# Kernel optimization log

Measured on AMD Instinct MI355X. Metric: run time of the kernel, lower is better.

## Reference

```python
import jax, jax.numpy as jnp
import numpy as np

B, T, H, L = 256, 1024, 64, 5  # batch, seq_len, hidden_size, num_layers


def setup_inputs() -> dict:
    key = jax.random.key(0)
    ks = jax.random.split(key, 10)
    s = 1.0 / np.sqrt(H)  # PyTorch LSTM/Linear uniform init bound

    def u(k, shape):
        return jax.random.uniform(k, shape, jnp.float32, -s, s)

    return {
        "x": jax.random.normal(ks[0], (B, T, 1), jnp.float32),
        "w_ih0": u(ks[1], (4 * H, 1)),          # layer 0 input weights (input_size=1)
        "w_ih_rest": u(ks[2], (L - 1, 4 * H, H)),  # layers 1..4 input weights
        "w_hh": u(ks[3], (L, 4 * H, H)),
        "b_ih": u(ks[4], (L, 4 * H)),
        "b_hh": u(ks[5], (L, 4 * H)),
        "W1": u(ks[6], (H, H)),
        "b1": u(ks[7], (H,)),
        "W2": u(ks[8], (1, H)),
        "b2": u(ks[9], (1,)),
        "future": 0,
    }


def _lstm_layer(x, w_ih, w_hh, b_ih, b_hh):
    # x: [B, T, in]; PyTorch gate order i, f, g, o
    gx = jnp.einsum('bti,gi->btg', x, w_ih) + b_ih  # precompute input projections [B,T,4H]
    h0 = jnp.zeros((x.shape[0], w_hh.shape[1]), x.dtype)

    def step(carry, gxt):
        h, c = carry
        gates = gxt + h @ w_hh.T + b_hh  # [B,4H]
        i, f, g, o = jnp.split(gates, 4, axis=-1)
        c = jax.nn.sigmoid(f) * c + jax.nn.sigmoid(i) * jnp.tanh(g)
        h = jax.nn.sigmoid(o) * jnp.tanh(c)
        return (h, c), h

    _, hs = jax.lax.scan(step, (h0, h0), jnp.swapaxes(gx, 0, 1))  # scan over time
    return jnp.swapaxes(hs, 0, 1)  # [B,T,H]


def _model(x, w_ih0, w_ih_rest, w_hh, b_ih, b_hh, W1, b1, W2, b2):
    # 5-layer LSTM (inter-layer dropout=0.1 is inactive in eval mode)
    h = _lstm_layer(x, w_ih0, w_hh[0], b_ih[0], b_hh[0])
    for l in range(1, w_hh.shape[0]):
        h = _lstm_layer(h, w_ih_rest[l - 1], w_hh[l], b_ih[l], b_hh[l])
    h = jax.nn.relu(h)
    h = jax.nn.relu(h @ W1.T + b1)
    return h @ W2.T + b2  # [B,T,1]


def reference(x, w_ih0, w_ih_rest, w_hh, b_ih, b_hh, W1, b1, W2, b2, future):
    out = None
    for _ in range(future + 1):
        out = _model(x, w_ih0, w_ih_rest, w_hh, b_ih, b_hh, W1, b1, W2, b2)
        x = jnp.concatenate([x, out[:, -1:, :]], axis=1)
    return out
```

## Files before the change

### kernel.cpp

```cpp
#include <hip/hip_runtime.h>

#define B_ 256
#define T_ 1024
#define H_ 64

typedef float f32x2 __attribute__((ext_vector_type(2)));
typedef float f32x4 __attribute__((ext_vector_type(4)));

__device__ __forceinline__ float fast_tanh(float x) {
    float e = __builtin_amdgcn_exp2f(2.8853900817779268f * x);
    return 1.0f - 2.0f * __builtin_amdgcn_rcpf(1.0f + e);
}

template<int CTRL>
__device__ __forceinline__ float dpp_addf(float v) {
    int vi = __builtin_bit_cast(int, v);
    int sh = __builtin_amdgcn_update_dpp(0, vi, CTRL, 0xF, 0xF, true);
    return v + __builtin_bit_cast(float, sh);
}
template<int CTRL>
__device__ __forceinline__ float dpp_movf(float v) {
    int vi = __builtin_bit_cast(int, v);
    int sh = __builtin_amdgcn_update_dpp(0, vi, CTRL, 0xF, 0xF, true);
    return __builtin_bit_cast(float, sh);
}

__device__ __forceinline__ void block_sync_lds() {
    asm volatile("s_waitcnt lgkmcnt(0)\n\ts_barrier" ::: "memory");
}

__device__ __forceinline__ float hsum4(f32x4 v) { return (v.x + v.y) + (v.z + v.w); }

__device__ __forceinline__ void gate_acts(const float acc[4], float bias_,
                                          float xterm, int kc,
                                          float& act, float& fv, float& gv, float& ov) {
    float acc_lo = (kc & 1) ? acc[1] : acc[0];
    float acc_hi = (kc & 1) ? acc[3] : acc[2];
    float pre = ((kc & 2) ? acc_hi : acc_lo) + bias_ + xterm;
    const bool isg = (kc == 2);
    float kk = isg ? 2.8853900817779268f : -1.4426950408889634f;
    float e = __builtin_amdgcn_exp2f(kk * pre);
    float r = __builtin_amdgcn_rcpf(1.0f + e);
    act = isg ? 1.0f - 2.0f * r : r;
    fv = dpp_movf<0xB1>(act);
    gv = dpp_movf<0x4E>(act);
    ov = dpp_movf<0x4E>(fv);
}

__device__ __forceinline__ void load_w_heavy(const float* __restrict__ w_ih,
                                             const float* __restrict__ w_hh,
                                             int j, int kc, f32x4 wt[4][8]) {
    #pragma unroll
    for (int r = 0; r < 4; ++r) {
        const int row = r * H_ + j;
        const float* base = (kc < 2) ? (w_ih + row * H_ + kc * 32)
                                     : (w_hh + row * H_ + (kc - 2) * 32);
        #pragma unroll
        for (int q = 0; q < 8; ++q)
            wt[r][q] = *(const f32x4*)(base + 4 * q);
    }
    #pragma unroll
    for (int r = 0; r < 4; ++r)
        #pragma unroll
        for (int q = 0; q < 8; ++q)
            asm volatile("" : "+v"(wt[r][q]));
}

__device__ __forceinline__ void dot4x32(const float* chunk, const f32x4 wt[4][8],
                                        float acc[4]) {
    const f32x4* xv = (const f32x4*)chunk;
    f32x4 a0 = {0,0,0,0}, a1 = {0,0,0,0}, a2 = {0,0,0,0}, a3 = {0,0,0,0};
    #pragma unroll
    for (int q = 0; q < 8; ++q) {
        f32x4 hq = xv[q];
        a0 = __builtin_elementwise_fma(wt[0][q], hq, a0);
        a1 = __builtin_elementwise_fma(wt[1][q], hq, a1);
        a2 = __builtin_elementwise_fma(wt[2][q], hq, a2);
        a3 = __builtin_elementwise_fma(wt[3][q], hq, a3);
    }
    acc[0] = hsum4(a0); acc[1] = hsum4(a1);
    acc[2] = hsum4(a2); acc[3] = hsum4(a3);
}

__global__ __launch_bounds__(768, 3)
void lstm_tri012(const float* __restrict__ x,
                 float* __restrict__ hout,
                 const float* __restrict__ w_ih0,
                 const float* __restrict__ whh0,
                 const float* __restrict__ bih0, const float* __restrict__ bhh0,
                 const float* __restrict__ wih1, const float* __restrict__ whh1,
                 const float* __restrict__ bih1, const float* __restrict__ bhh1,
                 const float* __restrict__ wih2, const float* __restrict__ whh2,
                 const float* __restrict__ bih2, const float* __restrict__ bhh2)
{
    const int b    = blockIdx.x;
    const int tid  = threadIdx.x;
    const int role = tid >> 8;
    const int loc  = tid & 255;
    const int kc   = loc & 3;
    const int j    = loc >> 2;

    __shared__ __align__(16) float bufL0[2][80];
    __shared__ __align__(16) float bufL1[2][144];
    __shared__ __align__(16) float bufL2[2][144];

    f32x4 wt[4][8];
    float bias_ = 0.f;
    float w0_   = 0.f;

    if (role == 0) {
        #pragma unroll
        for (int r = 0; r < 4; ++r) {
            const int row = r * H_ + j;
            const float* base = whh0 + row * H_ + kc * 16;
            #pragma unroll
            for (int q = 0; q < 4; ++q)
                wt[r][q] = *(const f32x4*)(base + 4 * q);
        }
        #pragma unroll
        for (int r = 0; r < 4; ++r)
            #pragma unroll
            for (int q = 0; q < 4; ++q)
                asm volatile("" : "+v"(wt[r][q]));
        bias_ = bih0[kc*H_+j] + bhh0[kc*H_+j];
        w0_   = w_ih0[kc*H_+j];
    } else {
        const float* wih = (role == 1) ? wih1 : wih2;
        const float* whh = (role == 1) ? whh1 : whh2;
        const float* bih = (role == 1) ? bih1 : bih2;
        const float* bhh = (role == 1) ? bhh1 : bhh2;
        load_w_heavy(wih, whh, j, kc, wt);
        bias_ = bih[kc*H_+j] + bhh[kc*H_+j];
    }
    float c_st = 0.f;
    float xt = (role == 0) ? x[(long)b * T_] : 0.f;

    float (*myBuf)[144] = (role == 1) ? bufL1 : bufL2;

    if (loc < H_) {
        const int u = loc;
        if (role == 0)      bufL0[0][(u >> 4) * 20 + (u & 15)] = 0.f;
        else if (role == 1) bufL1[1][(2 + (u >> 5)) * 36 + (u & 31)] = 0.f;
        else                bufL2[0][(2 + (u >> 5)) * 36 + (u & 31)] = 0.f;
    }
    block_sync_lds();

    #pragma unroll 2
    for (int s = 0; s <= T_ + 1; ++s) {
        const int rb = s & 1, wb = rb ^ 1;
        const bool active = (role == 0) ? (s < T_)
                          : (role == 1) ? (s >= 1 && s <= T_)
                                        : (s >= 2);
        if (active) {
            if (role == 0) {
                float xn = 0.f;
                if (s + 1 < T_) xn = x[(long)b * T_ + s + 1];
                const f32x4* xv = (const f32x4*)&bufL0[rb][kc * 20];
                f32x4 h0 = xv[0], h1 = xv[1], h2 = xv[2], h3 = xv[3];
                f32x4 a0 = {0,0,0,0}, a1 = {0,0,0,0}, a2 = {0,0,0,0}, a3 = {0,0,0,0};
                a0 = __builtin_elementwise_fma(wt[0][0], h0, a0);
                a1 = __builtin_elementwise_fma(wt[1][0], h0, a1);
                a2 = __builtin_elementwise_fma(wt[2][0], h0, a2);
                a3 = __builtin_elementwise_fma(wt[3][0], h0, a3);
                a0 = __builtin_elementwise_fma(wt[0][1], h1, a0);
                a1 = __builtin_elementwise_fma(wt[1][1], h1, a1);
                a2 = __builtin_elementwise_fma(wt[2][1], h1, a2);
                a3 = __builtin_elementwise_fma(wt[3][1], h1, a3);
                a0 = __builtin_elementwise_fma(wt[0][2], h2, a0);
                a1 = __builtin_elementwise_fma(wt[1][2], h2, a1);
                a2 = __builtin_elementwise_fma(wt[2][2], h2, a2);
                a3 = __builtin_elementwise_fma(wt[3][2], h2, a3);
                a0 = __builtin_elementwise_fma(wt[0][3], h3, a0);
                a1 = __builtin_elementwise_fma(wt[1][3], h3, a1);
                a2 = __builtin_elementwise_fma(wt[2][3], h3, a2);
                a3 = __builtin_elementwise_fma(wt[3][3], h3, a3);
                float acc[4];
                acc[0] = hsum4(a0); acc[1] = hsum4(a1);
                acc[2] = hsum4(a2); acc[3] = hsum4(a3);
                acc[0] = dpp_addf<0xB1>(acc[0]); acc[1] = dpp_addf<0xB1>(acc[1]);
                acc[2] = dpp_addf<0xB1>(acc[2]); acc[3] = dpp_addf<0xB1>(acc[3]);
                acc[0] = dpp_addf<0x4E>(acc[0]); acc[1] = dpp_addf<0x4E>(acc[1]);
                acc[2] = dpp_addf<0x4E>(acc[2]); acc[3] = dpp_addf<0x4E>(acc[3]);
                float act, fv, gv, ov;
                gate_acts(acc, bias_, w0_ * xt, kc, act, fv, gv, ov);
                if (kc == 0) {
                    c_st = fv * c_st + act * gv;
                    float h = ov * fast_tanh(c_st);
                    bufL0[wb][(j >> 4) * 20 + (j & 15)] = h;
                    bufL1[wb][(j >> 5) * 36 + (j & 31)] = h;
                }
                xt = xn;
            } else {
                float acc[4];
                dot4x32(&myBuf[rb][kc * 36], wt, acc);
                acc[0] = dpp_addf<0xB1>(acc[0]); acc[1] = dpp_addf<0xB1>(acc[1]);
                acc[2] = dpp_addf<0xB1>(acc[2]); acc[3] = dpp_addf<0xB1>(acc[3]);
                acc[0] = dpp_addf<0x4E>(acc[0]); acc[1] = dpp_addf<0x4E>(acc[1]);
                acc[2] = dpp_addf<0x4E>(acc[2]); acc[3] = dpp_addf<0x4E>(acc[3]);
                float act, fv, gv, ov;
                gate_acts(acc, bias_, 0.f, kc, act, fv, gv, ov);
                if (kc == 0) {
                    c_st = fv * c_st + act * gv;
                    float h = ov * fast_tanh(c_st);
                    myBuf[wb][(2 + (j >> 5)) * 36 + (j & 31)] = h;
                    if (role == 1)
                        bufL2[wb][(j >> 5) * 36 + (j & 31)] = h;
                    else
                        hout[((long)b * T_ + (s - 2)) * H_ + j] = h;
                }
            }
        }
        block_sync_lds();
    }
}

__global__ __launch_bounds__(512, 2)
void lstm_pair34(const float* __restrict__ xin,
                 float* __restrict__ hout,
                 const float* __restrict__ wih3, const float* __restrict__ whh3,
                 const float* __restrict__ bih3, const float* __restrict__ bhh3,
                 const float* __restrict__ wih4, const float* __restrict__ whh4,
                 const float* __restrict__ bih4, const float* __restrict__ bhh4)
{
    const int b    = blockIdx.x;
    const int tid  = threadIdx.x;
    const int role = tid >> 8;
    const int loc  = tid & 255;
    const int kc   = loc & 3;
    const int j    = loc >> 2;

    __shared__ __align__(16) float bufL3[2][144];
    __shared__ __align__(16) float bufL4[2][144];

    const float* wih = (role == 0) ? wih3 : wih4;
    const float* whh = (role == 0) ? whh3 : whh4;
    const float* bih = (role == 0) ? bih3 : bih4;
    const float* bhh = (role == 0) ? bhh3 : bhh4;
    float (*myBuf)[144] = (role == 0) ? bufL3 : bufL4;

    f32x4 wt[4][8];
    load_w_heavy(wih, whh, j, kc, wt);

    float bias_ = bih[kc*H_+j] + bhh[kc*H_+j];
    float c_st = 0.f;

    if (tid < H_) {
        const int u = tid;
        bufL3[0][(u >> 5) * 36 + (u & 31)] = xin[(long)b * T_ * H_ + u];
        bufL3[0][(2 + (u >> 5)) * 36 + (u & 31)] = 0.f;
    } else if (tid < 128) {
        const int u = tid - 64;
        bufL4[1][(2 + (u >> 5)) * 36 + (u & 31)] = 0.f;
    }
    block_sync_lds();

    #pragma unroll 2
    for (int s = 0; s <= T_; ++s) {
        const int rb = s & 1, wb = rb ^ 1;
        const bool active = (role == 0) ? (s < T_) : (s >= 1);
        if (active) {
            float xn = 0.f;
            if (role == 0 && kc == 1 && s + 1 < T_)
                xn = xin[((long)b * T_ + s + 1) * H_ + j];

            float acc[4];
            dot4x32(&myBuf[rb][kc * 36], wt, acc);
            acc[0] = dpp_addf<0xB1>(acc[0]); acc[1] = dpp_addf<0xB1>(acc[1]);
            acc[2] = dpp_addf<0xB1>(acc[2]); acc[3] = dpp_addf<0xB1>(acc[3]);
            acc[0] = dpp_addf<0x4E>(acc[0]); acc[1] = dpp_addf<0x4E>(acc[1]);
            acc[2] = dpp_addf<0x4E>(acc[2]); acc[3] = dpp_addf<0x4E>(acc[3]);

            float act, fv, gv, ov;
            gate_acts(acc, bias_, 0.f, kc, act, fv, gv, ov);
            if (kc == 0) {
                c_st = fv * c_st + act * gv;
                float h = ov * fast_tanh(c_st);
                myBuf[wb][(2 + (j >> 5)) * 36 + (j & 31)] = h;
                if (role == 0)
                    bufL4[wb][(j >> 5) * 36 + (j & 31)] = h;
                else
                    hout[((long)b * T_ + (s - 1)) * H_ + j] = h;
            }
            if (role == 0 && kc == 1)
                bufL3[wb][(j >> 5) * 36 + (j & 31)] = xn;
        }
        block_sync_lds();
    }
}

__global__ __launch_bounds__(256)
void mlp_head_v2(const float* __restrict__ hbuf,
                 const float* __restrict__ W1,
                 const float* __restrict__ b1,
                 const float* __restrict__ W2,
                 const float* __restrict__ b2,
                 float* __restrict__ out)
{
    const long r = (long)blockIdx.x * 256 + threadIdx.x;

    float row[H_];
    const float4* src = (const float4*)(hbuf + r * H_);
    #pragma unroll
    for (int q = 0; q < 16; ++q) {
        float4 v = src[q];
        row[4*q+0] = fmaxf(v.x, 0.f); row[4*q+1] = fmaxf(v.y, 0.f);
        row[4*q+2] = fmaxf(v.z, 0.f); row[4*q+3] = fmaxf(v.w, 0.f);
    }
    #pragma unroll
    for (int q = 0; q < 16; ++q)
        asm volatile("" : "+v"(row[4*q]), "+v"(row[4*q+1]),
                         "+v"(row[4*q+2]), "+v"(row[4*q+3]));

    float acc = b2[0];
    for (int jj = 0; jj < H_; ++jj) {
        const float* wrow = W1 + jj * H_;
        float s0 = 0.f, s1 = 0.f, s2 = 0.f, s3 = 0.f;
        #pragma unroll
        for (int q = 0; q < 16; ++q) {
            s0 += row[4*q+0] * wrow[4*q+0];
            s1 += row[4*q+1] * wrow[4*q+1];
            s2 += row[4*q+2] * wrow[4*q+2];
            s3 += row[4*q+3] * wrow[4*q+3];
        }
        float y = fmaxf(b1[jj] + (s0 + s1) + (s2 + s3), 0.f);
        acc += y * W2[jj];
    }
    out[r] = acc;
}

extern "C" void kernel_launch(void* const* d_in, const int* in_sizes, int n_in,
                              void* d_out, int out_size, void* d_ws, size_t ws_size,
                              hipStream_t stream) {
    const float* x     = (const float*)d_in[0];
    const float* w_ih0 = (const float*)d_in[1];
    const float* w_ihr = (const float*)d_in[2];
    const float* w_hh  = (const float*)d_in[3];
    const float* b_ih  = (const float*)d_in[4];
    const float* b_hh  = (const float*)d_in[5];
    const float* W1    = (const float*)d_in[6];
    const float* b1    = (const float*)d_in[7];
    const float* W2    = (const float*)d_in[8];
    const float* b2    = (const float*)d_in[9];

    float* out = (float*)d_out;
    float* buf = (float*)d_ws;

    const long LW = 4L * H_ * H_;
    const long LB = 4L * H_;

    lstm_tri012<<<dim3(B_), dim3(768), 0, stream>>>(
        x, buf,
        w_ih0, w_hh + 0 * LW, b_ih + 0 * LB, b_hh + 0 * LB,
        w_ihr + 0 * LW, w_hh + 1 * LW, b_ih + 1 * LB, b_hh + 1 * LB,
        w_ihr + 1 * LW, w_hh + 2 * LW, b_ih + 2 * LB, b_hh + 2 * LB);

    lstm_pair34<<<dim3(B_), dim3(512), 0, stream>>>(
        buf, buf,
        w_ihr + 2 * LW, w_hh + 3 * LW, b_ih + 3 * LB, b_hh + 3 * LB,
        w_ihr + 3 * LW, w_hh + 4 * LW, b_ih + 4 * LB, b_hh + 4 * LB);

    mlp_head_v2<<<dim3((B_ * T_) / 256), dim3(256), 0, stream>>>(
        buf, W1, b1, W2, b2, out);
}
```

Baseline: 1.545 ms.

## Split each hidden unit across eight lanes in layer 3-4 LSTM kernel

```diff
diff --git a/kernel.cpp b/kernel.cpp
--- a/kernel.cpp
+++ b/kernel.cpp
@@ -32,12 +32,12 @@
 __device__ __forceinline__ float hsum4(f32x4 v) { return (v.x + v.y) + (v.z + v.w); }
 
 __device__ __forceinline__ void gate_acts(const float acc[4], float bias_,
-                                          float xterm, int kc,
+                                          float xterm, int km,
                                           float& act, float& fv, float& gv, float& ov) {
-    float acc_lo = (kc & 1) ? acc[1] : acc[0];
-    float acc_hi = (kc & 1) ? acc[3] : acc[2];
-    float pre = ((kc & 2) ? acc_hi : acc_lo) + bias_ + xterm;
-    const bool isg = (kc == 2);
+    float acc_lo = (km & 1) ? acc[1] : acc[0];
+    float acc_hi = (km & 1) ? acc[3] : acc[2];
+    float pre = ((km & 2) ? acc_hi : acc_lo) + bias_ + xterm;
+    const bool isg = (km == 2);
     float kk = isg ? 2.8853900817779268f : -1.4426950408889634f;
     float e = __builtin_amdgcn_exp2f(kk * pre);
     float r = __builtin_amdgcn_rcpf(1.0f + e);
@@ -72,6 +72,41 @@
     f32x4 a0 = {0,0,0,0}, a1 = {0,0,0,0}, a2 = {0,0,0,0}, a3 = {0,0,0,0};
     #pragma unroll
     for (int q = 0; q < 8; ++q) {
+        f32x4 hq = xv[q];
+        a0 = __builtin_elementwise_fma(wt[0][q], hq, a0);
+        a1 = __builtin_elementwise_fma(wt[1][q], hq, a1);
+        a2 = __builtin_elementwise_fma(wt[2][q], hq, a2);
+        a3 = __builtin_elementwise_fma(wt[3][q], hq, a3);
+    }
+    acc[0] = hsum4(a0); acc[1] = hsum4(a1);
+    acc[2] = hsum4(a2); acc[3] = hsum4(a3);
+}
+
+__device__ __forceinline__ void load_w_oct(const float* __restrict__ w_ih,
+                                           const float* __restrict__ w_hh,
+                                           int j, int kc, f32x4 wt[4][4]) {
+    #pragma unroll
+    for (int r = 0; r < 4; ++r) {
+        const int row = r * H_ + j;
+        const float* base = (kc < 4) ? (w_ih + row * H_ + kc * 16)
+                                     : (w_hh + row * H_ + (kc - 4) * 16);
+        #pragma unroll
+        for (int q = 0; q < 4; ++q)
+            wt[r][q] = *(const f32x4*)(base + 4 * q);
+    }
+    #pragma unroll
+    for (int r = 0; r < 4; ++r)
+        #pragma unroll
+        for (int q = 0; q < 4; ++q)
+            asm volatile("" : "+v"(wt[r][q]));
+}
+
+__device__ __forceinline__ void dot4x16(const float* chunk, const f32x4 wt[4][4],
+                                        float acc[4]) {
+    const f32x4* xv = (const f32x4*)chunk;
+    f32x4 a0 = {0,0,0,0}, a1 = {0,0,0,0}, a2 = {0,0,0,0}, a3 = {0,0,0,0};
+    #pragma unroll
+    for (int q = 0; q < 4; ++q) {
         f32x4 hq = xv[q];
         a0 = __builtin_elementwise_fma(wt[0][q], hq, a0);
         a1 = __builtin_elementwise_fma(wt[1][q], hq, a1);
@@ -214,7 +249,7 @@
     }
 }
 
-__global__ __launch_bounds__(512, 2)
+__global__ __launch_bounds__(1024, 4)
 void lstm_pair34(const float* __restrict__ xin,
                  float* __restrict__ hout,
                  const float* __restrict__ wih3, const float* __restrict__ whh3,
@@ -224,33 +259,34 @@
 {
     const int b    = blockIdx.x;
     const int tid  = threadIdx.x;
-    const int role = tid >> 8;
-    const int loc  = tid & 255;
-    const int kc   = loc & 3;
-    const int j    = loc >> 2;
-
-    __shared__ __align__(16) float bufL3[2][144];
-    __shared__ __align__(16) float bufL4[2][144];
+    const int role = tid >> 9;
+    const int loc  = tid & 511;
+    const int kc   = loc & 7;
+    const int km   = kc & 3;
+    const int j    = loc >> 3;
+
+    __shared__ __align__(16) float bufL3[2][160];
+    __shared__ __align__(16) float bufL4[2][160];
 
     const float* wih = (role == 0) ? wih3 : wih4;
     const float* whh = (role == 0) ? whh3 : whh4;
     const float* bih = (role == 0) ? bih3 : bih4;
     const float* bhh = (role == 0) ? bhh3 : bhh4;
-    float (*myBuf)[144] = (role == 0) ? bufL3 : bufL4;
-
-    f32x4 wt[4][8];
-    load_w_heavy(wih, whh, j, kc, wt);
-
-    float bias_ = bih[kc*H_+j] + bhh[kc*H_+j];
+    float (*myBuf)[160] = (role == 0) ? bufL3 : bufL4;
+
+    f32x4 wt[4][4];
+    load_w_oct(wih, whh, j, kc, wt);
+
+    float bias_ = bih[km*H_+j] + bhh[km*H_+j];
     float c_st = 0.f;
 
     if (tid < H_) {
         const int u = tid;
-        bufL3[0][(u >> 5) * 36 + (u & 31)] = xin[(long)b * T_ * H_ + u];
-        bufL3[0][(2 + (u >> 5)) * 36 + (u & 31)] = 0.f;
+        bufL3[0][(u >> 4) * 20 + (u & 15)] = xin[(long)b * T_ * H_ + u];
+        bufL3[0][(4 + (u >> 4)) * 20 + (u & 15)] = 0.f;
     } else if (tid < 128) {
         const int u = tid - 64;
-        bufL4[1][(2 + (u >> 5)) * 36 + (u & 31)] = 0.f;
+        bufL4[1][(4 + (u >> 4)) * 20 + (u & 15)] = 0.f;
     }
     block_sync_lds();
 
@@ -264,25 +300,27 @@
                 xn = xin[((long)b * T_ + s + 1) * H_ + j];
 
             float acc[4];
-            dot4x32(&myBuf[rb][kc * 36], wt, acc);
-            acc[0] = dpp_addf<0xB1>(acc[0]); acc[1] = dpp_addf<0xB1>(acc[1]);
-            acc[2] = dpp_addf<0xB1>(acc[2]); acc[3] = dpp_addf<0xB1>(acc[3]);
-            acc[0] = dpp_addf<0x4E>(acc[0]); acc[1] = dpp_addf<0x4E>(acc[1]);
-            acc[2] = dpp_addf<0x4E>(acc[2]); acc[3] = dpp_addf<0x4E>(acc[3]);
+            dot4x16(&myBuf[rb][kc * 20], wt, acc);
+            acc[0] = dpp_addf<0xB1>(acc[0]);  acc[1] = dpp_addf<0xB1>(acc[1]);
+            acc[2] = dpp_addf<0xB1>(acc[2]);  acc[3] = dpp_addf<0xB1>(acc[3]);
+            acc[0] = dpp_addf<0x4E>(acc[0]);  acc[1] = dpp_addf<0x4E>(acc[1]);
+            acc[2] = dpp_addf<0x4E>(acc[2]);  acc[3] = dpp_addf<0x4E>(acc[3]);
+            acc[0] = dpp_addf<0x141>(acc[0]); acc[1] = dpp_addf<0x141>(acc[1]);
+            acc[2] = dpp_addf<0x141>(acc[2]); acc[3] = dpp_addf<0x141>(acc[3]);
 
             float act, fv, gv, ov;
-            gate_acts(acc, bias_, 0.f, kc, act, fv, gv, ov);
+            gate_acts(acc, bias_, 0.f, km, act, fv, gv, ov);
             if (kc == 0) {
                 c_st = fv * c_st + act * gv;
                 float h = ov * fast_tanh(c_st);
-                myBuf[wb][(2 + (j >> 5)) * 36 + (j & 31)] = h;
+                myBuf[wb][(4 + (j >> 4)) * 20 + (j & 15)] = h;
                 if (role == 0)
-                    bufL4[wb][(j >> 5) * 36 + (j & 31)] = h;
+                    bufL4[wb][(j >> 4) * 20 + (j & 15)] = h;
                 else
                     hout[((long)b * T_ + (s - 1)) * H_ + j] = h;
             }
             if (role == 0 && kc == 1)
-                bufL3[wb][(j >> 5) * 36 + (j & 31)] = xn;
+                bufL3[wb][(j >> 4) * 20 + (j & 15)] = xn;
         }
         block_sync_lds();
     }
@@ -354,7 +392,7 @@
         w_ihr + 0 * LW, w_hh + 1 * LW, b_ih + 1 * LB, b_hh + 1 * LB,
         w_ihr + 1 * LW, w_hh + 2 * LW, b_ih + 2 * LB, b_hh + 2 * LB);
 
-    lstm_pair34<<<dim3(B_), dim3(512), 0, stream>>>(
+    lstm_pair34<<<dim3(B_), dim3(1024), 0, stream>>>(
         buf, buf,
         w_ihr + 2 * LW, w_hh + 3 * LW, b_ih + 3 * LB, b_hh + 3 * LB,
         w_ihr + 3 * LW, w_hh + 4 * LW, b_ih + 4 * LB, b_hh + 4 * LB);
```

After: 1.736 ms. +12.3%, slower.
